# Kernel tuning notes

Hardware: AMD Instinct MI355X
Metric: run time of the kernel (lower is better)

Reference implementation:

```python
import jax, jax.numpy as jnp
import numpy as np

FP8_MAX = 448.0  # max finite value of float8_e4m3fn
F8 = jnp.float8_e4m3fn


def setup_inputs() -> dict:
    key = jax.random.key(0)
    kx, kw, kb = jax.random.split(key, 3)
    B, S, K, N = 4, 2048, 4096, 16384
    x = jax.random.normal(kx, (B, S, K), dtype=jnp.float32)
    # Pre-quantized symmetric per-tensor FP8 weight: simulate quantization of a
    # realistically initialized fp32 weight with scale ws.
    ws = jnp.float32(0.01)
    w_fp32 = jax.random.normal(kw, (N, K), dtype=jnp.float32) * 0.02
    weight = jnp.clip(w_fp32 / ws, -FP8_MAX, FP8_MAX).astype(F8)  # [N, K] fp8
    weight_scale = jnp.full((1,), ws, dtype=jnp.float32)  # per-tensor strategy
    bias = jax.random.normal(kb, (N,), dtype=jnp.float32) * 0.01
    return {"x": x, "weight": weight, "weight_scale": weight_scale, "bias": bias}


def reference(x, weight, weight_scale, bias):
    # Dynamic per-tensor fp8 quantization of the activation (torchao
    # _input_activation_quant_func_fp8 with PerTensor granularity):
    # (input_scale * weight_scale), plus bias.
    amax = jnp.max(jnp.abs(x))
    x_scale = jnp.maximum(amax, jnp.float32(1e-12)) / FP8_MAX
    xq = jnp.clip(x / x_scale, -FP8_MAX, FP8_MAX).astype(F8).astype(jnp.float32)
    w = weight.astype(jnp.float32)  # [N, K]
    out = jnp.einsum("bsk,nk->bsn", xq, w)  # [B, S, N]
    out = out * (x_scale * weight_scale[0]) + bias
    return out
```

## Files before the change

kernel.cpp:

```cpp
#include <hip/hip_runtime.h>
#include <hip/hip_fp8.h>
#include <hip/hip_fp16.h>
#include <stdint.h>

#define FP8_MAX_V 448.0f

typedef float f32x16 __attribute__((ext_vector_type(16)));
typedef int i32x4 __attribute__((ext_vector_type(4)));
typedef int i32x8 __attribute__((ext_vector_type(8)));

__device__ __forceinline__ uint8_t cvt_fp8(float v) {
    return __hip_cvt_float_to_fp8(fminf(fmaxf(v, -FP8_MAX_V), FP8_MAX_V),
                                  __HIP_SATFINITE, __HIP_E4M3);
}

__global__ void fp8lin_init(unsigned* amax_bits) {
    *amax_bits = 0u;
}

__global__ void fp8lin_amax(const float4* __restrict__ x, unsigned* __restrict__ amax_bits, long n4) {
    float m = 0.f;
    long stride = (long)gridDim.x * blockDim.x;
    for (long i = blockIdx.x * (long)blockDim.x + threadIdx.x; i < n4; i += stride) {
        float4 v = x[i];
        m = fmaxf(m, fmaxf(fmaxf(fabsf(v.x), fabsf(v.y)), fmaxf(fabsf(v.z), fabsf(v.w))));
    }
#pragma unroll
    for (int o = 32; o; o >>= 1) m = fmaxf(m, __shfl_xor(m, o));
    if ((threadIdx.x & 63) == 0) atomicMax(amax_bits, __float_as_uint(m));
}

__global__ void fp8lin_scales(const unsigned* __restrict__ amax_bits,
                              const float* __restrict__ wscale,
                              float* __restrict__ scales) {
    float xs = fmaxf(__uint_as_float(*amax_bits), 1e-12f) / FP8_MAX_V;
    scales[0] = xs;
    scales[1] = xs * wscale[0];
}

__global__ void fp8lin_probe(const uint32_t* __restrict__ w, unsigned* __restrict__ flag) {
    __shared__ unsigned s32, s16, s4;
    if (threadIdx.x == 0) { s32 = 0u; s16 = 0u; s4 = 0u; }
    __syncthreads();
    unsigned o32 = 0u, o16 = 0u, o4 = 0u;
    for (int i = threadIdx.x; i < 4096; i += 256) {
        uint32_t v = w[i];
        o32 |= v & 0x000FFFFFu;
        uint32_t h0 = v & 0xFFFFu, h1 = v >> 16;
        o16 |= (h0 & 0x7Fu) | (h1 & 0x7Fu);
        o4  |= (h0 & 0x0Fu) | (h1 & 0x0Fu);
    }
    atomicOr(&s32, o32); atomicOr(&s16, o16); atomicOr(&s4, o4);
    __syncthreads();
    if (threadIdx.x == 0)
        *flag = (s32 == 0u) ? 0u : (s16 == 0u) ? 1u : (s4 == 0u) ? 2u : 3u;
}

__global__ void fp8lin_convw(const void* __restrict__ wsrc, const unsigned* __restrict__ flag,
                             uchar4* __restrict__ wq, long n4) {
    unsigned f = *flag;
    if (f == 3u) return;
    long stride = (long)gridDim.x * blockDim.x;
    if (f == 0u) {
        const float4* src = (const float4*)wsrc;
        for (long i = blockIdx.x * (long)blockDim.x + threadIdx.x; i < n4; i += stride) {
            float4 v = src[i];
            uchar4 o;
            o.x = cvt_fp8(v.x); o.y = cvt_fp8(v.y); o.z = cvt_fp8(v.z); o.w = cvt_fp8(v.w);
            wq[i] = o;
        }
    } else if (f == 1u) {
        const __half2* src = (const __half2*)wsrc;
        for (long i = blockIdx.x * (long)blockDim.x + threadIdx.x; i < n4; i += stride) {
            __half2 v0 = src[2 * i], v1 = src[2 * i + 1];
            uchar4 o;
            o.x = cvt_fp8(__half2float(v0.x)); o.y = cvt_fp8(__half2float(v0.y));
            o.z = cvt_fp8(__half2float(v1.x)); o.w = cvt_fp8(__half2float(v1.y));
            wq[i] = o;
        }
    } else {
        const ushort2* src = (const ushort2*)wsrc;
        for (long i = blockIdx.x * (long)blockDim.x + threadIdx.x; i < n4; i += stride) {
            ushort2 v0 = src[2 * i], v1 = src[2 * i + 1];
            uchar4 o;
            o.x = cvt_fp8(__uint_as_float((uint32_t)v0.x << 16));
            o.y = cvt_fp8(__uint_as_float((uint32_t)v0.y << 16));
            o.z = cvt_fp8(__uint_as_float((uint32_t)v1.x << 16));
            o.w = cvt_fp8(__uint_as_float((uint32_t)v1.y << 16));
            wq[i] = o;
        }
    }
}

__global__ void fp8lin_quant(const float4* __restrict__ x, const float* __restrict__ scales,
                             uchar4* __restrict__ xq, long n4) {
    float s = scales[0];
    long stride = (long)gridDim.x * blockDim.x;
    for (long i = blockIdx.x * (long)blockDim.x + threadIdx.x; i < n4; i += stride) {
        float4 v = x[i];
        uchar4 o;
        o.x = cvt_fp8(v.x / s); o.y = cvt_fp8(v.y / s);
        o.z = cvt_fp8(v.z / s); o.w = cvt_fp8(v.w / s);
        xq[i] = o;
    }
}

#define BM 256
#define BN 256
#define BK 64
#define TILE_BYTES 16384
#define BUF_BYTES (2 * TILE_BYTES)
#define SMEM_BYTES (2 * BUF_BYTES)

__device__ __forceinline__ void gload16(const uint8_t* src, uint8_t* ldst) {
    __builtin_amdgcn_global_load_lds(
        (const __attribute__((address_space(1))) uint32_t*)(uintptr_t)src,
        (__attribute__((address_space(3))) uint32_t*)(uintptr_t)ldst, 16, 0, 0);
}

#define WAITVM(N) asm volatile("s_waitcnt vmcnt(" #N ")" ::: "memory")
#define BARRIER() do { asm volatile("" ::: "memory"); __builtin_amdgcn_s_barrier(); \
                       asm volatile("" ::: "memory"); } while (0)

#define LDFRAG(dst, base, off) do {                                    \
    i32x4 _lo = *(const i32x4*)((base) + (off));                       \
    i32x4 _hi = *(const i32x4*)((base) + ((off) ^ 16));                \
    dst[0] = _lo[0]; dst[1] = _lo[1]; dst[2] = _lo[2]; dst[3] = _lo[3];\
    dst[4] = _hi[0]; dst[5] = _hi[1]; dst[6] = _hi[2]; dst[7] = _hi[3];\
} while (0)

#define MFMA_MX(A, B, C) __builtin_amdgcn_mfma_scale_f32_32x32x64_f8f6f4( \
    (A), (B), (C), 0, 0, 0, (int)0x7f7f7f7f, 0, (int)0x7f7f7f7f)

__global__ __launch_bounds__(512, 2) void fp8lin_gemm(
    const uint8_t* __restrict__ Aq,
    const uint8_t* __restrict__ Wraw,
    const uint8_t* __restrict__ Wconv,
    const unsigned* __restrict__ flag,
    const float* __restrict__ scales,
    const float* __restrict__ bias,
    float* __restrict__ out,
    int M, int N, int K) {
    extern __shared__ __align__(16) uint8_t smem[];

    const uint8_t* __restrict__ Wq = (*flag == 3u) ? Wraw : Wconv;

    const int tid = threadIdx.x;
    const int wid = tid >> 6;
    const int lane = tid & 63;
    const int wm = wid >> 2;
    const int wn = wid & 3;

    const int nbx = gridDim.x;
    const int orig = blockIdx.y * nbx + blockIdx.x;
    const int cpx = (gridDim.x * gridDim.y) >> 3;
    const int swzb = (orig & 7) * cpx + (orig >> 3);
    const int brow = (swzb / nbx) * BM;
    const int bcol = (swzb % nbx) * BN;

    const int c0 = tid, c1 = tid + 512;
    const int rS0 = c0 >> 2, rS1 = c1 >> 2;
    const int scS0 = ((c0 & 3) ^ ((rS0 >> 1) & 3)) * 16;
    const int scS1 = ((c1 & 3) ^ ((rS1 >> 1) & 3)) * 16;
    const uint8_t* srcA0 = Aq + (size_t)(brow + rS0) * K + scS0;
    const uint8_t* srcA1 = Aq + (size_t)(brow + rS1) * K + scS1;
    const uint8_t* srcB0 = Wq + (size_t)(bcol + rS0) * K + scS0;
    const uint8_t* srcB1 = Wq + (size_t)(bcol + rS1) * K + scS1;
    const int ldsJ0 = wid * 1024;
    const int ldsJ1 = wid * 1024 + 8192;

    const int l31 = lane & 31;
    const int q = lane >> 5;
    const int swzr = (l31 >> 1) & 3;
    const int posl = (2 * q) ^ swzr;
    const int offA = (wm * 128 + l31) * 64 + posl * 16;
    const int offB = (wn * 64 + l31) * 64 + posl * 16;

    f32x16 acc[4][2];
#pragma unroll
    for (int mi = 0; mi < 4; ++mi)
#pragma unroll
        for (int ni = 0; ni < 2; ++ni)
#pragma unroll
            for (int r = 0; r < 16; ++r) acc[mi][ni][r] = 0.0f;

    auto STAGE = [&](int t, int ib) {
        size_t k0 = (size_t)t * BK;
        uint8_t* base = smem + ib * BUF_BYTES;
        gload16(srcA0 + k0, base + ldsJ0);
        gload16(srcA1 + k0, base + ldsJ1);
        gload16(srcB0 + k0, base + TILE_BYTES + ldsJ0);
        gload16(srcB1 + k0, base + TILE_BYTES + ldsJ1);
    };

    auto COMPUTE = [&](int ib) {
        const uint8_t* bA = smem + ib * BUF_BYTES;
        const uint8_t* bB = bA + TILE_BYTES;
        i32x8 a0, a1, a2, a3, b0, b1;
        LDFRAG(a0, bA, offA);
        LDFRAG(a1, bA, offA + 2048);
        LDFRAG(b0, bB, offB);
        LDFRAG(b1, bB, offB + 2048);
        __builtin_amdgcn_s_setprio(1);
        acc[0][0] = MFMA_MX(a0, b0, acc[0][0]);
        acc[1][0] = MFMA_MX(a1, b0, acc[1][0]);
        acc[0][1] = MFMA_MX(a0, b1, acc[0][1]);
        acc[1][1] = MFMA_MX(a1, b1, acc[1][1]);
        __builtin_amdgcn_s_setprio(0);
        LDFRAG(a2, bA, offA + 4096);
        LDFRAG(a3, bA, offA + 6144);
        __builtin_amdgcn_s_setprio(1);
        acc[2][0] = MFMA_MX(a2, b0, acc[2][0]);
        acc[3][0] = MFMA_MX(a3, b0, acc[3][0]);
        acc[2][1] = MFMA_MX(a2, b1, acc[2][1]);
        acc[3][1] = MFMA_MX(a3, b1, acc[3][1]);
        __builtin_amdgcn_s_setprio(0);
    };

    const int NT = K / BK;
    STAGE(0, 0);
    int cur = 0;
    for (int t = 0; t < NT - 1; ++t) {
        STAGE(t + 1, cur ^ 1);
        WAITVM(4);
        BARRIER();
        COMPUTE(cur);
        BARRIER();
        cur ^= 1;
    }
    WAITVM(0);
    BARRIER();
    COMPUTE(cur);

    float s = scales[1];
    const int colg = bcol + wn * 64 + l31;
    const int rowg0 = brow + wm * 128 + 4 * q;
#pragma unroll
    for (int ni = 0; ni < 2; ++ni) {
        int col = colg + ni * 32;
        float bv = bias[col];
#pragma unroll
        for (int mi = 0; mi < 4; ++mi) {
            int rb = rowg0 + mi * 32;
#pragma unroll
            for (int reg = 0; reg < 16; ++reg) {
                int row = rb + (reg & 3) + 8 * (reg >> 2);
                __builtin_nontemporal_store(acc[mi][ni][reg] * s + bv,
                                            out + (size_t)row * N + col);
            }
        }
    }
}

extern "C" void kernel_launch(void* const* d_in, const int* in_sizes, int n_in,
                              void* d_out, int out_size, void* d_ws, size_t ws_size,
                              hipStream_t stream) {
    const float* x = (const float*)d_in[0];
    const void* w = d_in[1];
    const float* wscale = (const float*)d_in[2];
    const float* bias = (const float*)d_in[3];
    float* out = (float*)d_out;

    const int Bb = 4, S = 2048, K = 4096, N = 16384;
    const int M = Bb * S;
    const long nx = (long)M * K;
    const long nw = (long)N * K;

    unsigned* amax_bits = (unsigned*)d_ws;
    float* scales = (float*)((char*)d_ws + 16);
    unsigned* wflag = (unsigned*)((char*)d_ws + 32);
    uchar4* xq = (uchar4*)((char*)d_ws + 256);
    uchar4* wq = (uchar4*)((char*)d_ws + 256 + nx);

    fp8lin_init<<<1, 1, 0, stream>>>(amax_bits);
    fp8lin_probe<<<1, 256, 0, stream>>>((const uint32_t*)w, wflag);
    fp8lin_amax<<<2048, 256, 0, stream>>>((const float4*)x, amax_bits, nx / 4);
    fp8lin_scales<<<1, 1, 0, stream>>>(amax_bits, wscale, scales);
    fp8lin_quant<<<2048, 256, 0, stream>>>((const float4*)x, scales, xq, nx / 4);
    fp8lin_convw<<<2048, 256, 0, stream>>>(w, wflag, wq, nw / 4);

    dim3 grid(N / BN, M / BM);
    fp8lin_gemm<<<grid, 512, SMEM_BYTES, stream>>>((const uint8_t*)xq, (const uint8_t*)w,
                                                   (const uint8_t*)wq, wflag, scales, bias, out,
                                                   M, N, K);
}
```

Measured before the change: 793.8 us.

## Shrink GEMM block tile to 256x128 with 4 waves per block

Halves the N dimension of the block tile from 256 to 128 and the workgroup from 8 to 4 waves, keeping each wave's 128x64 sub-tile. Staging now issues six 16-byte LDS loads per thread per k-step, and the vmcnt wait is adjusted to match. The smaller shared-memory footprint and block size should allow more resident blocks and twice as many of them in the grid. In exchange, the A tile is reused across fewer columns, so more global and L2 traffic goes to A.

```diff
diff --git a/kernel.cpp b/kernel.cpp
--- a/kernel.cpp
+++ b/kernel.cpp
@@ -106,10 +106,11 @@
 }
 
 #define BM 256
-#define BN 256
+#define BN 128
 #define BK 64
-#define TILE_BYTES 16384
-#define BUF_BYTES (2 * TILE_BYTES)
+#define A_BYTES 16384
+#define B_BYTES 8192
+#define BUF_BYTES (A_BYTES + B_BYTES)
 #define SMEM_BYTES (2 * BUF_BYTES)
 
 __device__ __forceinline__ void gload16(const uint8_t* src, uint8_t* ldst) {
@@ -132,7 +133,7 @@
 #define MFMA_MX(A, B, C) __builtin_amdgcn_mfma_scale_f32_32x32x64_f8f6f4( \
     (A), (B), (C), 0, 0, 0, (int)0x7f7f7f7f, 0, (int)0x7f7f7f7f)
 
-__global__ __launch_bounds__(512, 2) void fp8lin_gemm(
+__global__ __launch_bounds__(256, 2) void fp8lin_gemm(
     const uint8_t* __restrict__ Aq,
     const uint8_t* __restrict__ Wraw,
     const uint8_t* __restrict__ Wconv,
@@ -148,8 +149,8 @@
     const int tid = threadIdx.x;
     const int wid = tid >> 6;
     const int lane = tid & 63;
-    const int wm = wid >> 2;
-    const int wn = wid & 3;
+    const int wm = wid >> 1;
+    const int wn = wid & 1;
 
     const int nbx = gridDim.x;
     const int orig = blockIdx.y * nbx + blockIdx.x;
@@ -158,16 +159,23 @@
     const int brow = (swzb / nbx) * BM;
     const int bcol = (swzb % nbx) * BN;
 
-    const int c0 = tid, c1 = tid + 512;
-    const int rS0 = c0 >> 2, rS1 = c1 >> 2;
-    const int scS0 = ((c0 & 3) ^ ((rS0 >> 1) & 3)) * 16;
-    const int scS1 = ((c1 & 3) ^ ((rS1 >> 1) & 3)) * 16;
-    const uint8_t* srcA0 = Aq + (size_t)(brow + rS0) * K + scS0;
-    const uint8_t* srcA1 = Aq + (size_t)(brow + rS1) * K + scS1;
-    const uint8_t* srcB0 = Wq + (size_t)(bcol + rS0) * K + scS0;
-    const uint8_t* srcB1 = Wq + (size_t)(bcol + rS1) * K + scS1;
-    const int ldsJ0 = wid * 1024;
-    const int ldsJ1 = wid * 1024 + 8192;
+    const uint8_t* srcA[4];
+    const uint8_t* srcB[2];
+#pragma unroll
+    for (int j = 0; j < 4; ++j) {
+        int c = tid + 256 * j;
+        int r = c >> 2;
+        int sc = ((c & 3) ^ ((r >> 1) & 3)) * 16;
+        srcA[j] = Aq + (size_t)(brow + r) * K + sc;
+    }
+#pragma unroll
+    for (int j = 0; j < 2; ++j) {
+        int c = tid + 256 * j;
+        int r = c >> 2;
+        int sc = ((c & 3) ^ ((r >> 1) & 3)) * 16;
+        srcB[j] = Wq + (size_t)(bcol + r) * K + sc;
+    }
+    const int ldsW = wid * 1024;
 
     const int l31 = lane & 31;
     const int q = lane >> 5;
@@ -187,15 +195,17 @@
     auto STAGE = [&](int t, int ib) {
         size_t k0 = (size_t)t * BK;
         uint8_t* base = smem + ib * BUF_BYTES;
-        gload16(srcA0 + k0, base + ldsJ0);
-        gload16(srcA1 + k0, base + ldsJ1);
-        gload16(srcB0 + k0, base + TILE_BYTES + ldsJ0);
-        gload16(srcB1 + k0, base + TILE_BYTES + ldsJ1);
+        gload16(srcA[0] + k0, base + ldsW);
+        gload16(srcA[1] + k0, base + ldsW + 4096);
+        gload16(srcA[2] + k0, base + ldsW + 8192);
+        gload16(srcA[3] + k0, base + ldsW + 12288);
+        gload16(srcB[0] + k0, base + A_BYTES + ldsW);
+        gload16(srcB[1] + k0, base + A_BYTES + ldsW + 4096);
     };
 
     auto COMPUTE = [&](int ib) {
         const uint8_t* bA = smem + ib * BUF_BYTES;
-        const uint8_t* bB = bA + TILE_BYTES;
+        const uint8_t* bB = bA + A_BYTES;
         i32x8 a0, a1, a2, a3, b0, b1;
         LDFRAG(a0, bA, offA);
         LDFRAG(a1, bA, offA + 2048);
@@ -222,7 +232,7 @@
     int cur = 0;
     for (int t = 0; t < NT - 1; ++t) {
         STAGE(t + 1, cur ^ 1);
-        WAITVM(4);
+        WAITVM(6);
         BARRIER();
         COMPUTE(cur);
         BARRIER();
@@ -280,7 +290,7 @@
     fp8lin_convw<<<2048, 256, 0, stream>>>(w, wflag, wq, nw / 4);
 
     dim3 grid(N / BN, M / BM);
-    fp8lin_gemm<<<grid, 512, SMEM_BYTES, stream>>>((const uint8_t*)xq, (const uint8_t*)w,
+    fp8lin_gemm<<<grid, 256, SMEM_BYTES, stream>>>((const uint8_t*)xq, (const uint8_t*)w,
                                                    (const uint8_t*)wq, wflag, scales, bias, out,
                                                    M, N, K);
 }
```

After: 778.5 us. Within noise of the previous version (-1.9%).

## Use triple-buffered LDS pipeline with interleaved global loads and MFMA phases

Applied to the files above, without the earlier changes.

Replaces the double-buffered K-loop with a three-stage LDS ring that prefetches two tiles ahead. The four global-to-LDS loads per tile are spread across four MFMA phases, each fenced by barriers and lgkmcnt waits, in a ping-pong style schedule. The load mapping changes so each wave fills contiguous 1KB chunks. The goal is to hide global memory latency and keep issue pressure even, at the cost of more LDS per block (96KB), which may limit occupancy to fewer blocks per CU, and more barriers per iteration.

```diff
diff --git a/kernel.cpp b/kernel.cpp
--- a/kernel.cpp
+++ b/kernel.cpp
@@ -108,9 +108,10 @@
 #define BM 256
 #define BN 256
 #define BK 64
-#define TILE_BYTES 16384
-#define BUF_BYTES (2 * TILE_BYTES)
-#define SMEM_BYTES (2 * BUF_BYTES)
+#define A_TILE 16384
+#define B_TILE 16384
+#define BUF_BYTES (A_TILE + B_TILE)
+#define SMEM_BYTES (3 * BUF_BYTES)
 
 __device__ __forceinline__ void gload16(const uint8_t* src, uint8_t* ldst) {
     __builtin_amdgcn_global_load_lds(
@@ -119,6 +120,8 @@
 }
 
 #define WAITVM(N) asm volatile("s_waitcnt vmcnt(" #N ")" ::: "memory")
+#define LGKM0() do { asm volatile("s_waitcnt lgkmcnt(0)" ::: "memory"); \
+                     __builtin_amdgcn_sched_barrier(0); } while (0)
 #define BARRIER() do { asm volatile("" ::: "memory"); __builtin_amdgcn_s_barrier(); \
                        asm volatile("" ::: "memory"); } while (0)
 
@@ -158,16 +161,16 @@
     const int brow = (swzb / nbx) * BM;
     const int bcol = (swzb % nbx) * BN;
 
-    const int c0 = tid, c1 = tid + 512;
-    const int rS0 = c0 >> 2, rS1 = c1 >> 2;
-    const int scS0 = ((c0 & 3) ^ ((rS0 >> 1) & 3)) * 16;
-    const int scS1 = ((c1 & 3) ^ ((rS1 >> 1) & 3)) * 16;
-    const uint8_t* srcA0 = Aq + (size_t)(brow + rS0) * K + scS0;
-    const uint8_t* srcA1 = Aq + (size_t)(brow + rS1) * K + scS1;
-    const uint8_t* srcB0 = Wq + (size_t)(bcol + rS0) * K + scS0;
-    const uint8_t* srcB1 = Wq + (size_t)(bcol + rS1) * K + scS1;
-    const int ldsJ0 = wid * 1024;
-    const int ldsJ1 = wid * 1024 + 8192;
+    const int ca0 = wid * 2, ca1 = wid * 2 + 1;
+    const int rA0 = ca0 * 16 + (lane >> 2), rA1 = ca1 * 16 + (lane >> 2);
+    const int gA0 = ((lane & 3) ^ ((rA0 >> 1) & 3)) * 16;
+    const int gA1 = ((lane & 3) ^ ((rA1 >> 1) & 3)) * 16;
+    const uint8_t* sA0 = Aq + (size_t)(brow + rA0) * K + gA0;
+    const uint8_t* sA1 = Aq + (size_t)(brow + rA1) * K + gA1;
+    const uint8_t* sB0 = Wq + (size_t)(bcol + rA0) * K + gA0;
+    const uint8_t* sB1 = Wq + (size_t)(bcol + rA1) * K + gA1;
+    const int dA0 = ca0 * 1024, dA1 = ca1 * 1024;
+    const int dB0 = A_TILE + ca0 * 1024, dB1 = A_TILE + ca1 * 1024;
 
     const int l31 = lane & 31;
     const int q = lane >> 5;
@@ -184,53 +187,70 @@
 #pragma unroll
             for (int r = 0; r < 16; ++r) acc[mi][ni][r] = 0.0f;
 
-    auto STAGE = [&](int t, int ib) {
-        size_t k0 = (size_t)t * BK;
-        uint8_t* base = smem + ib * BUF_BYTES;
-        gload16(srcA0 + k0, base + ldsJ0);
-        gload16(srcA1 + k0, base + ldsJ1);
-        gload16(srcB0 + k0, base + TILE_BYTES + ldsJ0);
-        gload16(srcB1 + k0, base + TILE_BYTES + ldsJ1);
-    };
-
-    auto COMPUTE = [&](int ib) {
-        const uint8_t* bA = smem + ib * BUF_BYTES;
-        const uint8_t* bB = bA + TILE_BYTES;
+    {
+        uint8_t* b0 = smem;
+        uint8_t* b1 = smem + BUF_BYTES;
+        gload16(sA0, b0 + dA0); gload16(sA1, b0 + dA1);
+        gload16(sB0, b0 + dB0); gload16(sB1, b0 + dB1);
+        gload16(sA0 + BK, b1 + dA0); gload16(sA1 + BK, b1 + dA1);
+        gload16(sB0 + BK, b1 + dB0); gload16(sB1 + BK, b1 + dB1);
+        WAITVM(4);
+        BARRIER();
+    }
+
+    const int NT = K / BK;
+    int cur = 0;
+    for (int t = 0; t < NT; ++t) {
+        const uint8_t* bA = smem + cur * BUF_BYTES;
+        const uint8_t* bB = bA + A_TILE;
+        int nxt = cur + 2; if (nxt >= 3) nxt -= 3;
+        uint8_t* nb = smem + nxt * BUF_BYTES;
+        const bool st = (t + 2) < NT;
+        const size_t k2 = (size_t)(t + 2) * BK;
+
         i32x8 a0, a1, a2, a3, b0, b1;
         LDFRAG(a0, bA, offA);
         LDFRAG(a1, bA, offA + 2048);
         LDFRAG(b0, bB, offB);
-        LDFRAG(b1, bB, offB + 2048);
+        if (st) gload16(sA0 + k2, nb + dA0);
+        BARRIER();
+        LGKM0();
         __builtin_amdgcn_s_setprio(1);
         acc[0][0] = MFMA_MX(a0, b0, acc[0][0]);
         acc[1][0] = MFMA_MX(a1, b0, acc[1][0]);
+        __builtin_amdgcn_s_setprio(0);
+        BARRIER();
+        LDFRAG(b1, bB, offB + 2048);
+        if (st) gload16(sA1 + k2, nb + dA1);
+        BARRIER();
+        LGKM0();
+        __builtin_amdgcn_s_setprio(1);
         acc[0][1] = MFMA_MX(a0, b1, acc[0][1]);
         acc[1][1] = MFMA_MX(a1, b1, acc[1][1]);
         __builtin_amdgcn_s_setprio(0);
+        BARRIER();
         LDFRAG(a2, bA, offA + 4096);
         LDFRAG(a3, bA, offA + 6144);
+        if (st) gload16(sB0 + k2, nb + dB0);
+        BARRIER();
+        LGKM0();
         __builtin_amdgcn_s_setprio(1);
         acc[2][0] = MFMA_MX(a2, b0, acc[2][0]);
         acc[3][0] = MFMA_MX(a3, b0, acc[3][0]);
+        __builtin_amdgcn_s_setprio(0);
+        BARRIER();
+        if (st) gload16(sB1 + k2, nb + dB1);
+        BARRIER();
+        LGKM0();
+        __builtin_amdgcn_s_setprio(1);
         acc[2][1] = MFMA_MX(a2, b1, acc[2][1]);
         acc[3][1] = MFMA_MX(a3, b1, acc[3][1]);
         __builtin_amdgcn_s_setprio(0);
-    };
-
-    const int NT = K / BK;
-    STAGE(0, 0);
-    int cur = 0;
-    for (int t = 0; t < NT - 1; ++t) {
-        STAGE(t + 1, cur ^ 1);
-        WAITVM(4);
-        BARRIER();
-        COMPUTE(cur);
-        BARRIER();
-        cur ^= 1;
-    }
-    WAITVM(0);
-    BARRIER();
-    COMPUTE(cur);
+        if (t < NT - 2) { WAITVM(4); }
+        else if (t == NT - 2) { WAITVM(0); }
+        BARRIER();
+        ++cur; if (cur == 3) cur = 0;
+    }
 
     float s = scales[1];
     const int colg = bcol + wn * 64 + l31;
```

Measured after the change: 789.3 us. About the same (-0.6%).
